# Kernel optimization log

Hardware: AMD Instinct MI355X
Metric: run time of the kernel (lower is better)

Reference implementation:

```python
import jax, jax.numpy as jnp
import numpy as np

H = 90            # hidden_size (hard-coded in module)
NODE_F = 16       # conv1 in_channels = dim(x) + dim(pos)
EDGE_F = 8
N_GRAPHS = 512


def _init_linear(key, fan_in, fan_out):
    kw, kb = jax.random.split(key)
    bound = 1.0 / np.sqrt(fan_in)
    w = jax.random.uniform(kw, (fan_in, fan_out), minval=-bound, maxval=bound, dtype=jnp.float32)
    b = jax.random.uniform(kb, (fan_out,), minval=-bound, maxval=bound, dtype=jnp.float32)
    return w, b


def setup_inputs() -> dict:
    key = jax.random.key(0)
    ks = jax.random.split(key, 16)
    N, E = 16000, 64000
    x = jax.random.normal(ks[0], (N, 13), dtype=jnp.float32)
    pos = jax.random.normal(ks[1], (N, 3), dtype=jnp.float32)
    edge_attr = jax.random.normal(ks[2], (E, EDGE_F), dtype=jnp.float32)
    edge_index = jax.random.randint(ks[3], (2, E), 0, N, dtype=jnp.int32)
    batch = jnp.sort(jax.random.randint(ks[4], (N,), 0, N_GRAPHS, dtype=jnp.int32))

    # conv1: edge MLP edge_f -> H -> NODE_F*H ; root [NODE_F,H]; bias [H]
    c1_w1, c1_b1 = _init_linear(ks[5], EDGE_F, H)
    c1_w2, c1_b2 = _init_linear(ks[6], H, NODE_F * H)
    c1_root = jax.random.normal(ks[7], (NODE_F, H), dtype=jnp.float32) / np.sqrt(NODE_F)
    c1_bias = jnp.zeros((H,), dtype=jnp.float32)
    # conv2: H -> H
    c2_w1, c2_b1 = _init_linear(ks[8], EDGE_F, H)
    c2_w2, c2_b2 = _init_linear(ks[9], H, H * H)
    c2_root = jax.random.normal(ks[10], (H, H), dtype=jnp.float32) / np.sqrt(H)
    c2_bias = jnp.zeros((H,), dtype=jnp.float32)
    # conv3: H -> H//2
    c3_w1, c3_b1 = _init_linear(ks[11], EDGE_F, H)
    c3_w2, c3_b2 = _init_linear(ks[12], H, H * (H // 2))
    c3_root = jax.random.normal(ks[13], (H, H // 2), dtype=jnp.float32) / np.sqrt(H)
    c3_bias = jnp.zeros((H // 2,), dtype=jnp.float32)

    fc1_w, fc1_b = _init_linear(ks[14], H // 2, H)
    out_w, out_b = _init_linear(ks[15], H, 1)

    return dict(x=x, pos=pos, edge_attr=edge_attr, edge_index=edge_index, batch=batch,
                c1_w1=c1_w1, c1_b1=c1_b1, c1_w2=c1_w2, c1_b2=c1_b2, c1_root=c1_root, c1_bias=c1_bias,
                c2_w1=c2_w1, c2_b1=c2_b1, c2_w2=c2_w2, c2_b2=c2_b2, c2_root=c2_root, c2_bias=c2_bias,
                c3_w1=c3_w1, c3_b1=c3_b1, c3_w2=c3_w2, c3_b2=c3_b2, c3_root=c3_root, c3_bias=c3_bias,
                fc1_w=fc1_w, fc1_b=fc1_b, out_w=out_w, out_b=out_b)


def _nnconv(x, src, dst, edge_attr, w1, b1, w2, b2, root, bias, in_c, out_c):
    # edge MLP -> per-edge weight matrix theta[e] in R^{in_c x out_c}
    h = jax.nn.relu(edge_attr @ w1 + b1)                  # [E, H]
    theta = (h @ w2 + b2).reshape(-1, in_c, out_c)        # [E, in_c, out_c]
    msg = jnp.einsum('ei,eio->eo', x[src], theta)         # gather + per-edge matvec
    agg = jax.ops.segment_sum(msg, dst, num_segments=x.shape[0])  # scatter-add
    return agg + x @ root + bias


def reference(x, pos, edge_attr, edge_index, batch,
              c1_w1, c1_b1, c1_w2, c1_b2, c1_root, c1_bias,
              c2_w1, c2_b1, c2_w2, c2_b2, c2_root, c2_bias,
              c3_w1, c3_b1, c3_w2, c3_b2, c3_root, c3_bias,
              fc1_w, fc1_b, out_w, out_b):
    src, dst = edge_index[0], edge_index[1]
    h = jnp.concatenate([x, pos], axis=1)                 # [N, NODE_F]
    h = jax.nn.relu(_nnconv(h, src, dst, edge_attr, c1_w1, c1_b1, c1_w2, c1_b2, c1_root, c1_bias, NODE_F, H))
    h = jax.nn.relu(_nnconv(h, src, dst, edge_attr, c2_w1, c2_b1, c2_w2, c2_b2, c2_root, c2_bias, H, H))
    h = jax.nn.relu(_nnconv(h, src, dst, edge_attr, c3_w1, c3_b1, c3_w2, c3_b2, c3_root, c3_bias, H, H // 2))
    g = jax.ops.segment_sum(h, batch, num_segments=N_GRAPHS)  # global_add_pool
    g = jax.nn.relu(g @ fc1_w + fc1_b)
    return g @ out_w + out_b                               # [N_GRAPHS, 1]
```

## Files before the change

### kernel.cpp

```cpp
#include <hip/hip_runtime.h>

#define NN 16000
#define NE 64000
#define HD 90
#define NG 512

typedef float f32x4 __attribute__((ext_vector_type(4)));
typedef short s16x8 __attribute__((ext_vector_type(8)));

__device__ __forceinline__ unsigned short rhu1(float f) {
  return (unsigned short)((__builtin_bit_cast(unsigned int, f) + 0x8000u) >> 16);
}
__device__ __forceinline__ unsigned int rhu_pack(float lo, float hi) {
  unsigned int ul = __builtin_bit_cast(unsigned int, lo) + 0x8000u;
  unsigned int uh = __builtin_bit_cast(unsigned int, hi) + 0x8000u;
  return __builtin_amdgcn_perm(uh, ul, 0x07060302u);
}
__device__ __forceinline__ float bfhi(unsigned int u) {
  return __builtin_bit_cast(float, u & 0xFFFF0000u);
}
__device__ __forceinline__ float bflo(unsigned int u) {
  return __builtin_bit_cast(float, u << 16);
}

__global__ void concat_kernel(const float* __restrict__ x, const float* __restrict__ pos,
                              float* __restrict__ h0) {
  int idx = blockIdx.x * 256 + threadIdx.x;
  if (idx >= NN * 16) return;
  int n = idx >> 4, c = idx & 15;
  h0[idx] = (c < 13) ? x[n * 13 + c] : pos[n * 3 + (c - 13)];
}

__global__ void edge_mlp_bf(const float* __restrict__ ea, const float* __restrict__ w1,
                            const float* __restrict__ b1, unsigned short* __restrict__ he) {
  int idx = blockIdx.x * 256 + threadIdx.x;
  if (idx >= NE * 96) return;
  int e = idx / 96, k = idx - e * 96;
  unsigned short v;
  if (k < 90) {
    const float* a = ea + e * 8;
    float acc = b1[k];
#pragma unroll
    for (int j = 0; j < 8; j++) acc = fmaf(a[j], w1[j * HD + k], acc);
    v = rhu1(fmaxf(acc, 0.f));
  } else {
    v = (k == 90) ? (unsigned short)0x3F80 : (unsigned short)0;
  }
  he[idx] = v;
}

template <int OC, int NTT>
__global__ void wprep_frag(const float* __restrict__ w2, const float* __restrict__ b2,
                           unsigned short* __restrict__ wout, int inc_oc) {
  const int i = blockIdx.x / 3, c = blockIdx.x - 3 * (blockIdx.x / 3);
  __shared__ float t_s[32 * 100];
  const int tid = threadIdx.x;
  for (int idx = tid; idx < 32 * 96; idx += 256) {
    int kk = idx / 96, o = idx - kk * 96;
    int hk = c * 32 + kk;
    float v = 0.f;
    if (o < OC) {
      if (hk < 90) v = w2[hk * inc_oc + i * OC + o];
      else if (hk == 90) v = b2[i * OC + o];
    }
    t_s[kk * 100 + o] = v;
  }
  __syncthreads();
  unsigned int* wo = (unsigned int*)(wout + (size_t)i * NTT * 3 * 512) + c * 256;
  for (int idx = tid; idx < NTT * 256; idx += 256) {
    int t = idx >> 8, r = idx & 255;
    int lane = r >> 2, u = r & 3;
    int kk = (lane >> 4) * 8 + 2 * u;
    int o = t * 16 + (lane & 15);
    wo[(size_t)t * 3 * 256 + lane * 4 + u] = rhu_pack(t_s[kk * 100 + o], t_s[(kk + 1) * 100 + o]);
  }
}

template <int ILIM, int OC, int NTT, int NWG, int EPB, int BLK>
__global__ __launch_bounds__(BLK, 4)
void msg_mfma(const unsigned short* __restrict__ he,
              const float* __restrict__ nin,
              const int* __restrict__ src, const int* __restrict__ dst,
              const unsigned short* __restrict__ wp,
              float* __restrict__ agg) {
  constexpr int WMG = EPB / 32;
  constexpr int TPE = BLK / EPB;
  constexpr int NWAVES = BLK / 64;
  constexpr int NF = NTT * 3;
  __shared__ unsigned short zb[ILIM * WMG * 32];
  __shared__ unsigned short wbuf[2][NF * 512];
  __shared__ int dst_s[EPB];
  const int tid = threadIdx.x;
  const int e0 = blockIdx.x * EPB;
  const int wid = tid >> 6, l = tid & 63, ln = tid & 15, q = (tid & 63) >> 4;
  const int wn = wid % NWG, wm = wid / NWG;
  const int eb = wm * 32;
  const int wn3 = wn * 3;

  const unsigned short* wl = wp + l * 8;
  auto stage = [&](int ii, int buf) {
#pragma unroll
    for (int t = 0; t < (NF + NWAVES - 1) / NWAVES; t++) {
      const int s = wid + t * NWAVES;
      if (s < NF) {
        __builtin_amdgcn_global_load_lds(
            (const __attribute__((address_space(1))) unsigned int*)(wl + ((size_t)ii * NF + s) * 512),
            (__attribute__((address_space(3))) unsigned int*)&wbuf[buf][s * 512],
            16, 0, 0);
      }
    }
  };

  stage(0, 0);

  if (tid < EPB) dst_s[tid] = dst[e0 + tid];

  {
    const int e = tid % EPB, jj = tid / EPB;
    const int base = (e >> 5) * 32 + (((e & 15) >> 2) << 3) + (((e >> 4) & 1) << 2) + (e & 3);
    const float* zr = nin + (size_t)src[e0 + e] * ILIM;
    for (int p = jj; p < ILIM / 2; p += TPE) {
      const float2 v = *(const float2*)(zr + 2 * p);
      zb[(2 * p) * (WMG * 32) + base] = rhu1(v.x);
      zb[(2 * p + 1) * (WMG * 32) + base] = rhu1(v.y);
    }
  }

  s16x8 af[2][3];
#pragma unroll
  for (int mt = 0; mt < 2; mt++) {
    const unsigned short* hr = he + (size_t)(e0 + eb + mt * 16 + ln) * 96 + q * 8;
#pragma unroll
    for (int c = 0; c < 3; c++) af[mt][c] = *(const s16x8*)(hr + c * 32);
  }

  __syncthreads();

  f32x4 acc[2][3];
#pragma unroll
  for (int mt = 0; mt < 2; mt++)
#pragma unroll
    for (int nt = 0; nt < 3; nt++) acc[mt][nt] = (f32x4)0.f;

#pragma clang loop unroll(disable)
  for (int i = 0; i < ILIM; i++) {
    const int cur = i & 1;
    if (i + 1 < ILIM) stage(i + 1, cur ^ 1);

    const uint4 zu = *(const uint4*)&zb[(i * WMG + wm) * 32 + q * 8];
    f32x4 zv0, zv1;
    zv0[0] = bflo(zu.x); zv0[1] = bfhi(zu.x); zv0[2] = bflo(zu.y); zv0[3] = bfhi(zu.y);
    zv1[0] = bflo(zu.z); zv1[1] = bfhi(zu.z); zv1[2] = bflo(zu.w); zv1[3] = bfhi(zu.w);

    uint4 ba[9];
#pragma unroll
    for (int ntl = 0; ntl < 3; ntl++)
#pragma unroll
      for (int c = 0; c < 3; c++)
        ba[ntl * 3 + c] = *(const uint4*)&wbuf[cur][((wn3 + ntl) * 3 + c) * 512 + l * 8];

#pragma unroll
    for (int ntl = 0; ntl < 3; ntl++) {
      f32x4 t0 = __builtin_amdgcn_mfma_f32_16x16x32_bf16(af[0][0], __builtin_bit_cast(s16x8, ba[ntl * 3 + 0]), (f32x4)0.f, 0, 0, 0);
      t0 = __builtin_amdgcn_mfma_f32_16x16x32_bf16(af[0][1], __builtin_bit_cast(s16x8, ba[ntl * 3 + 1]), t0, 0, 0, 0);
      t0 = __builtin_amdgcn_mfma_f32_16x16x32_bf16(af[0][2], __builtin_bit_cast(s16x8, ba[ntl * 3 + 2]), t0, 0, 0, 0);
      f32x4 t1 = __builtin_amdgcn_mfma_f32_16x16x32_bf16(af[1][0], __builtin_bit_cast(s16x8, ba[ntl * 3 + 0]), (f32x4)0.f, 0, 0, 0);
      t1 = __builtin_amdgcn_mfma_f32_16x16x32_bf16(af[1][1], __builtin_bit_cast(s16x8, ba[ntl * 3 + 1]), t1, 0, 0, 0);
      t1 = __builtin_amdgcn_mfma_f32_16x16x32_bf16(af[1][2], __builtin_bit_cast(s16x8, ba[ntl * 3 + 2]), t1, 0, 0, 0);
      acc[0][ntl] += zv0 * t0;
      acc[1][ntl] += zv1 * t1;
    }

    if (i + 1 < ILIM) __syncthreads();
  }

#pragma unroll
  for (int mt = 0; mt < 2; mt++) {
#pragma unroll
    for (int ntl = 0; ntl < 3; ntl++) {
      int o = wn * 48 + ntl * 16 + ln;
      if (o < OC) {
#pragma unroll
        for (int r = 0; r < 4; r++) {
          int el = eb + mt * 16 + q * 4 + r;
          atomicAdd(agg + (size_t)dst_s[el] * OC + o, acc[mt][ntl][r]);
        }
      }
    }
  }
}

template <int IN_C, int OC>
__global__ void node_kernel(const float* __restrict__ agg, const float* __restrict__ nin,
                            const float* __restrict__ root, const float* __restrict__ bias,
                            float* __restrict__ out) {
  int idx = blockIdx.x * 256 + threadIdx.x;
  if (idx >= NN * OC) return;
  int n = idx / OC, o = idx - n * OC;
  float acc = agg[idx] + bias[o];
  const float* inp = nin + (size_t)n * IN_C;
#pragma unroll 6
  for (int i = 0; i < IN_C; i++) acc = fmaf(inp[i], root[i * OC + o], acc);
  out[idx] = fmaxf(acc, 0.f);
}

__global__ void pool_mlp_kernel(const float* __restrict__ h3, const int* __restrict__ batch,
                                const float* __restrict__ fc1_w, const float* __restrict__ fc1_b,
                                const float* __restrict__ out_w, const float* __restrict__ out_b,
                                float* __restrict__ out) {
  const int b = blockIdx.x;
  const int tid = threadIdx.x;
  __shared__ float g[45];
  __shared__ float go[90];
  __shared__ int rng[2];
  if (tid < 2) {
    int target = b + tid;
    int lo = 0, hi = NN;
    while (lo < hi) { int mid = (lo + hi) >> 1; if (batch[mid] < target) lo = mid + 1; else hi = mid; }
    rng[tid] = lo;
  }
  __syncthreads();
  const int s = rng[0], e = rng[1];
  if (tid < 45) {
    float acc = 0.f;
    for (int n = s; n < e; n++) acc += h3[n * 45 + tid];
    g[tid] = acc;
  }
  __syncthreads();
  if (tid < 90) {
    float acc = fc1_b[tid];
#pragma unroll 5
    for (int i = 0; i < 45; i++) acc = fmaf(g[i], fc1_w[i * 90 + tid], acc);
    go[tid] = fmaxf(acc, 0.f) * out_w[tid];
  }
  __syncthreads();
  if (tid == 0) {
    float acc = out_b[0];
    for (int i = 0; i < 90; i++) acc += go[i];
    out[b] = acc;
  }
}

extern "C" void kernel_launch(void* const* d_in, const int* in_sizes, int n_in,
                              void* d_out, int out_size, void* d_ws, size_t ws_size,
                              hipStream_t stream) {
  const float* x       = (const float*)d_in[0];
  const float* pos     = (const float*)d_in[1];
  const float* ea      = (const float*)d_in[2];
  const int*   eidx    = (const int*)d_in[3];
  const int*   batch   = (const int*)d_in[4];
  const float* c1_w1   = (const float*)d_in[5];
  const float* c1_b1   = (const float*)d_in[6];
  const float* c1_w2   = (const float*)d_in[7];
  const float* c1_b2   = (const float*)d_in[8];
  const float* c1_root = (const float*)d_in[9];
  const float* c1_bias = (const float*)d_in[10];
  const float* c2_w1   = (const float*)d_in[11];
  const float* c2_b1   = (const float*)d_in[12];
  const float* c2_w2   = (const float*)d_in[13];
  const float* c2_b2   = (const float*)d_in[14];
  const float* c2_root = (const float*)d_in[15];
  const float* c2_bias = (const float*)d_in[16];
  const float* c3_w1   = (const float*)d_in[17];
  const float* c3_b1   = (const float*)d_in[18];
  const float* c3_w2   = (const float*)d_in[19];
  const float* c3_b2   = (const float*)d_in[20];
  const float* c3_root = (const float*)d_in[21];
  const float* c3_bias = (const float*)d_in[22];
  const float* fc1_w   = (const float*)d_in[23];
  const float* fc1_b   = (const float*)d_in[24];
  const float* out_w   = (const float*)d_in[25];
  const float* out_b   = (const float*)d_in[26];
  const int* src = eidx;
  const int* dst = eidx + NE;

  float* ws  = (float*)d_ws;
  float* h0  = ws;
  float* h1  = h0 + NN * 16;
  float* h2  = h1 + NN * 90;
  float* h3  = h2 + NN * 90;
  float* agg = h3 + NN * 45;
  unsigned short* he_bf = (unsigned short*)(agg + NN * 90);
  unsigned short* wp1 = he_bf + (size_t)NE * 96;
  unsigned short* wp2 = wp1 + (size_t)16 * 6 * 3 * 512;
  unsigned short* wp3 = wp2 + (size_t)90 * 6 * 3 * 512;

  concat_kernel<<<(NN * 16) / 256, 256, 0, stream>>>(x, pos, h0);

  wprep_frag<90, 6><<<16 * 3, 256, 0, stream>>>(c1_w2, c1_b2, wp1, 16 * 90);
  wprep_frag<90, 6><<<90 * 3, 256, 0, stream>>>(c2_w2, c2_b2, wp2, 90 * 90);
  wprep_frag<45, 3><<<90 * 3, 256, 0, stream>>>(c3_w2, c3_b2, wp3, 90 * 45);

  hipMemsetAsync(agg, 0, (size_t)NN * 90 * sizeof(float), stream);
  edge_mlp_bf<<<(NE * 96) / 256, 256, 0, stream>>>(ea, c1_w1, c1_b1, he_bf);
  msg_mfma<16, 90, 6, 2, 128, 512><<<NE / 128, 512, 0, stream>>>(he_bf, h0, src, dst, wp1, agg);
  node_kernel<16, 90><<<(NN * 90) / 256, 256, 0, stream>>>(agg, h0, c1_root, c1_bias, h1);

  hipMemsetAsync(agg, 0, (size_t)NN * 90 * sizeof(float), stream);
  edge_mlp_bf<<<(NE * 96) / 256, 256, 0, stream>>>(ea, c2_w1, c2_b1, he_bf);
  msg_mfma<90, 90, 6, 2, 128, 512><<<NE / 128, 512, 0, stream>>>(he_bf, h1, src, dst, wp2, agg);
  node_kernel<90, 90><<<(NN * 90) / 256, 256, 0, stream>>>(agg, h1, c2_root, c2_bias, h2);

  hipMemsetAsync(agg, 0, (size_t)NN * 45 * sizeof(float), stream);
  edge_mlp_bf<<<(NE * 96) / 256, 256, 0, stream>>>(ea, c3_w1, c3_b1, he_bf);
  msg_mfma<90, 45, 3, 1, 128, 256><<<NE / 128, 256, 0, stream>>>(he_bf, h2, src, dst, wp3, agg);
  node_kernel<90, 45><<<(NN * 45 + 255) / 256, 256, 0, stream>>>(agg, h2, c3_root, c3_bias, h3);

  pool_mlp_kernel<<<NG, 128, 0, stream>>>(h3, batch, fc1_w, fc1_b, out_w, out_b, (float*)d_out);
}
```

Baseline: 549.2 us.

## Give each wave four edge M-tiles and halve block size in message MFMA kernel

Each wave in the message kernel now processes four 16-edge M-tiles instead of two. The number of waves per block is halved, so each weight fragment read from LDS feeds twice as many MFMAs and LDS traffic per FLOP drops. Launch bounds drop from 4 to 2 blocks, which allows more registers per thread for the larger accumulator and A-fragment arrays. The trade-off is fewer waves per block, which leaves less latency hiding, and fewer threads sharing the per-iteration weight staging. The staging pointer is also changed to an incrementing pointer.

New measurement: 561.6 us. 1.02x slower.

```diff
diff --git a/kernel.cpp b/kernel.cpp
--- a/kernel.cpp
+++ b/kernel.cpp
@@ -76,8 +76,8 @@
   }
 }
 
-template <int ILIM, int OC, int NTT, int NWG, int EPB, int BLK>
-__global__ __launch_bounds__(BLK, 4)
+template <int ILIM, int OC, int NTT, int NWG, int MT, int EPB, int BLK>
+__global__ __launch_bounds__(BLK, 2)
 void msg_mfma(const unsigned short* __restrict__ he,
               const float* __restrict__ nin,
               const int* __restrict__ src, const int* __restrict__ dst,
@@ -87,6 +87,7 @@
   constexpr int TPE = BLK / EPB;
   constexpr int NWAVES = BLK / 64;
   constexpr int NF = NTT * 3;
+  constexpr int MG = MT / 2;
   __shared__ unsigned short zb[ILIM * WMG * 32];
   __shared__ unsigned short wbuf[2][NF * 512];
   __shared__ int dst_s[EPB];
@@ -94,24 +95,25 @@
   const int e0 = blockIdx.x * EPB;
   const int wid = tid >> 6, l = tid & 63, ln = tid & 15, q = (tid & 63) >> 4;
   const int wn = wid % NWG, wm = wid / NWG;
-  const int eb = wm * 32;
+  const int eb = wm * MT * 16;
   const int wn3 = wn * 3;
 
   const unsigned short* wl = wp + l * 8;
-  auto stage = [&](int ii, int buf) {
+  auto stage = [&](const unsigned short* wb, int buf) {
 #pragma unroll
     for (int t = 0; t < (NF + NWAVES - 1) / NWAVES; t++) {
       const int s = wid + t * NWAVES;
       if (s < NF) {
         __builtin_amdgcn_global_load_lds(
-            (const __attribute__((address_space(1))) unsigned int*)(wl + ((size_t)ii * NF + s) * 512),
+            (const __attribute__((address_space(1))) unsigned int*)(wb + (size_t)s * 512),
             (__attribute__((address_space(3))) unsigned int*)&wbuf[buf][s * 512],
             16, 0, 0);
       }
     }
   };
 
-  stage(0, 0);
+  stage(wl, 0);
+  const unsigned short* wnext = wl + (size_t)NF * 512;
 
   if (tid < EPB) dst_s[tid] = dst[e0 + tid];
 
@@ -126,9 +128,9 @@
     }
   }
 
-  s16x8 af[2][3];
-#pragma unroll
-  for (int mt = 0; mt < 2; mt++) {
+  s16x8 af[MT][3];
+#pragma unroll
+  for (int mt = 0; mt < MT; mt++) {
     const unsigned short* hr = he + (size_t)(e0 + eb + mt * 16 + ln) * 96 + q * 8;
 #pragma unroll
     for (int c = 0; c < 3; c++) af[mt][c] = *(const s16x8*)(hr + c * 32);
@@ -136,21 +138,26 @@
 
   __syncthreads();
 
-  f32x4 acc[2][3];
-#pragma unroll
-  for (int mt = 0; mt < 2; mt++)
+  f32x4 acc[MT][3];
+#pragma unroll
+  for (int mt = 0; mt < MT; mt++)
 #pragma unroll
     for (int nt = 0; nt < 3; nt++) acc[mt][nt] = (f32x4)0.f;
 
 #pragma clang loop unroll(disable)
   for (int i = 0; i < ILIM; i++) {
     const int cur = i & 1;
-    if (i + 1 < ILIM) stage(i + 1, cur ^ 1);
-
-    const uint4 zu = *(const uint4*)&zb[(i * WMG + wm) * 32 + q * 8];
-    f32x4 zv0, zv1;
-    zv0[0] = bflo(zu.x); zv0[1] = bfhi(zu.x); zv0[2] = bflo(zu.y); zv0[3] = bfhi(zu.y);
-    zv1[0] = bflo(zu.z); zv1[1] = bfhi(zu.z); zv1[2] = bflo(zu.w); zv1[3] = bfhi(zu.w);
+    if (i + 1 < ILIM) { stage(wnext, cur ^ 1); wnext += (size_t)NF * 512; }
+
+    f32x4 zv[MT];
+#pragma unroll
+    for (int g = 0; g < MG; g++) {
+      const uint4 zu = *(const uint4*)&zb[(i * WMG + wm * MG + g) * 32 + q * 8];
+      zv[2 * g][0] = bflo(zu.x); zv[2 * g][1] = bfhi(zu.x);
+      zv[2 * g][2] = bflo(zu.y); zv[2 * g][3] = bfhi(zu.y);
+      zv[2 * g + 1][0] = bflo(zu.z); zv[2 * g + 1][1] = bfhi(zu.z);
+      zv[2 * g + 1][2] = bflo(zu.w); zv[2 * g + 1][3] = bfhi(zu.w);
+    }
 
     uint4 ba[9];
 #pragma unroll
@@ -161,21 +168,20 @@
 
 #pragma unroll
     for (int ntl = 0; ntl < 3; ntl++) {
-      f32x4 t0 = __builtin_amdgcn_mfma_f32_16x16x32_bf16(af[0][0], __builtin_bit_cast(s16x8, ba[ntl * 3 + 0]), (f32x4)0.f, 0, 0, 0);
-      t0 = __builtin_amdgcn_mfma_f32_16x16x32_bf16(af[0][1], __builtin_bit_cast(s16x8, ba[ntl * 3 + 1]), t0, 0, 0, 0);
-      t0 = __builtin_amdgcn_mfma_f32_16x16x32_bf16(af[0][2], __builtin_bit_cast(s16x8, ba[ntl * 3 + 2]), t0, 0, 0, 0);
-      f32x4 t1 = __builtin_amdgcn_mfma_f32_16x16x32_bf16(af[1][0], __builtin_bit_cast(s16x8, ba[ntl * 3 + 0]), (f32x4)0.f, 0, 0, 0);
-      t1 = __builtin_amdgcn_mfma_f32_16x16x32_bf16(af[1][1], __builtin_bit_cast(s16x8, ba[ntl * 3 + 1]), t1, 0, 0, 0);
-      t1 = __builtin_amdgcn_mfma_f32_16x16x32_bf16(af[1][2], __builtin_bit_cast(s16x8, ba[ntl * 3 + 2]), t1, 0, 0, 0);
-      acc[0][ntl] += zv0 * t0;
-      acc[1][ntl] += zv1 * t1;
+#pragma unroll
+      for (int mt = 0; mt < MT; mt++) {
+        f32x4 t = __builtin_amdgcn_mfma_f32_16x16x32_bf16(af[mt][0], __builtin_bit_cast(s16x8, ba[ntl * 3 + 0]), (f32x4)0.f, 0, 0, 0);
+        t = __builtin_amdgcn_mfma_f32_16x16x32_bf16(af[mt][1], __builtin_bit_cast(s16x8, ba[ntl * 3 + 1]), t, 0, 0, 0);
+        t = __builtin_amdgcn_mfma_f32_16x16x32_bf16(af[mt][2], __builtin_bit_cast(s16x8, ba[ntl * 3 + 2]), t, 0, 0, 0);
+        acc[mt][ntl] += zv[mt] * t;
+      }
     }
 
     if (i + 1 < ILIM) __syncthreads();
   }
 
 #pragma unroll
-  for (int mt = 0; mt < 2; mt++) {
+  for (int mt = 0; mt < MT; mt++) {
 #pragma unroll
     for (int ntl = 0; ntl < 3; ntl++) {
       int o = wn * 48 + ntl * 16 + ln;
@@ -293,17 +299,17 @@
 
   hipMemsetAsync(agg, 0, (size_t)NN * 90 * sizeof(float), stream);
   edge_mlp_bf<<<(NE * 96) / 256, 256, 0, stream>>>(ea, c1_w1, c1_b1, he_bf);
-  msg_mfma<16, 90, 6, 2, 128, 512><<<NE / 128, 512, 0, stream>>>(he_bf, h0, src, dst, wp1, agg);
+  msg_mfma<16, 90, 6, 2, 4, 128, 256><<<NE / 128, 256, 0, stream>>>(he_bf, h0, src, dst, wp1, agg);
   node_kernel<16, 90><<<(NN * 90) / 256, 256, 0, stream>>>(agg, h0, c1_root, c1_bias, h1);
 
   hipMemsetAsync(agg, 0, (size_t)NN * 90 * sizeof(float), stream);
   edge_mlp_bf<<<(NE * 96) / 256, 256, 0, stream>>>(ea, c2_w1, c2_b1, he_bf);
-  msg_mfma<90, 90, 6, 2, 128, 512><<<NE / 128, 512, 0, stream>>>(he_bf, h1, src, dst, wp2, agg);
+  msg_mfma<90, 90, 6, 2, 4, 128, 256><<<NE / 128, 256, 0, stream>>>(he_bf, h1, src, dst, wp2, agg);
   node_kernel<90, 90><<<(NN * 90) / 256, 256, 0, stream>>>(agg, h1, c2_root, c2_bias, h2);
 
   hipMemsetAsync(agg, 0, (size_t)NN * 45 * sizeof(float), stream);
   edge_mlp_bf<<<(NE * 96) / 256, 256, 0, stream>>>(ea, c3_w1, c3_b1, he_bf);
-  msg_mfma<90, 45, 3, 1, 128, 256><<<NE / 128, 256, 0, stream>>>(he_bf, h2, src, dst, wp3, agg);
+  msg_mfma<90, 45, 3, 1, 4, 128, 128><<<NE / 128, 128, 0, stream>>>(he_bf, h2, src, dst, wp3, agg);
   node_kernel<90, 45><<<(NN * 45 + 255) / 256, 256, 0, stream>>>(agg, h2, c3_root, c3_bias, h3);
 
   pool_mlp_kernel<<<NG, 128, 0, stream>>>(h3, batch, fc1_w, fc1_b, out_w, out_b, (float*)d_out);
```
